# Kernel tuning notes

Measured on AMD Instinct MI355X. Metric: run time of the kernel, lower is better.

## Reference

```python
import jax, jax.numpy as jnp
import numpy as np

N_NODES = 10000
N_EDGES = 320000
D_FEAT = 128          # per-node feature dim -> in_dim = 2*D_FEAT = 256
OUT_DIM = 128
SCALES = 3


def setup_inputs() -> dict:
    key = jax.random.key(0)
    ks = jax.random.split(key, 7)
    node_features = jax.random.normal(ks[0], (N_NODES, D_FEAT), dtype=jnp.float32)
    temporal_info = jax.random.normal(ks[1], (N_NODES,), dtype=jnp.float32)
    in_dim_p1 = 2 * D_FEAT + 1  # 257: concat(src, dest) + temporal gap
    W1 = jax.random.normal(ks[2], (SCALES, in_dim_p1, OUT_DIM), dtype=jnp.float32) * 0.05
    b1 = jax.random.normal(ks[3], (SCALES, OUT_DIM), dtype=jnp.float32) * 0.05
    W2 = jax.random.normal(ks[4], (SCALES, OUT_DIM, OUT_DIM), dtype=jnp.float32) * 0.05
    b2 = jax.random.normal(ks[5], (SCALES, OUT_DIM), dtype=jnp.float32) * 0.05
    edge_index = jax.random.randint(ks[6], (2, N_EDGES), 0, N_NODES, dtype=jnp.int64)
    return {
        "node_features": node_features,
        "temporal_info": temporal_info,
        "W1": W1, "b1": b1, "W2": W2, "b2": b2,
        "edge_index": edge_index,
    }


def reference(node_features, temporal_info, W1, b1, W2, b2, edge_index):
    src, dest = edge_index[0], edge_index[1]
    # gather node pairs + temporal gap -> [E, 2*D+1]
    gap = (temporal_info[src] - temporal_info[dest])[:, None]
    edge_features = jnp.concatenate(
        [node_features[src], node_features[dest], gap], axis=-1)
    # all scales' 2-layer MLPs in one batched einsum; s = scale axis
    h = jax.nn.relu(jnp.einsum('ef,sfo->seo', edge_features, W1) + b1[:, None, :])
    tokens = jnp.einsum('seo,sop->sep', h, W2) + b2[:, None, :]  # [S, E, OUT]
    return tokens.mean(axis=0)  # mean over scales -> [E, OUT]
```

## Files before the change

### kernel.cpp

```cpp
#include <hip/hip_runtime.h>
#include <stdint.h>

#define NN 10000
#define NE 320000
#define DF 128
#define OD 128
#define NS 3

typedef __attribute__((ext_vector_type(8))) short bf16x8;
typedef __attribute__((ext_vector_type(16))) float f32x16;

static __device__ __forceinline__ uint32_t f2bf(float f) {
  uint32_t u = __float_as_uint(f);
  return (u + 0x7FFFu + ((u >> 16) & 1u)) >> 16;
}
static __device__ __forceinline__ float bflo(uint32_t u) { return __uint_as_float(u << 16); }
static __device__ __forceinline__ float bfhi(uint32_t u) { return __uint_as_float(u & 0xFFFF0000u); }

static __device__ __forceinline__ uint32_t relu2(uint32_t a, uint32_t d) {
  float f0 = fmaxf(bflo(a) + bflo(d), 0.0f);
  float f1 = fmaxf(bfhi(a) + bfhi(d), 0.0f);
  return f2bf(f0) | (f2bf(f1) << 16);
}

__global__ __launch_bounds__(256) void prep_w2(
    const float* __restrict__ W2, const float* __restrict__ b2,
    unsigned short* __restrict__ w2t, float* __restrict__ bmean)
{
  int tid = blockIdx.x * 256 + threadIdx.x;
  if (tid < NS * OD * OD) {
    int s = tid / (OD * OD);
    int r = tid % (OD * OD);
    int k = r / OD;
    int n = r % OD;
    w2t[(s * OD + n) * OD + k] = (unsigned short)f2bf(W2[tid]);
  }
  if (tid < OD) bmean[tid] = (b2[tid] + b2[OD + tid] + b2[2 * OD + tid]) * (1.0f / 3.0f);
}

__global__ __launch_bounds__(256) void node_proj(
    const float* __restrict__ nf, const float* __restrict__ temporal,
    const float* __restrict__ W1, const float* __restrict__ b1,
    unsigned short* __restrict__ Qsrc, unsigned short* __restrict__ Qdst)
{
  __shared__ unsigned short Asm[8 * 64 * 8];
  __shared__ unsigned short Bsm[4 * 8 * 64 * 8];
  __shared__ float tsh[32];

  const int t = threadIdx.x;
  const int c = blockIdx.y;
  const int s = c >> 1, proj = c & 1;

  {
    int o = t & 127, qh = t >> 7;
    const float* wbase = W1 + (size_t)(s * 257 + proj * 128) * OD + o;
    int nt = o >> 5, lnlo = o & 31;
    #pragma unroll
    for (int r = 0; r < 8; r++) {
      int kh = qh * 8 + r;
      float v[8];
      #pragma unroll
      for (int j = 0; j < 8; j++) v[j] = wbase[(size_t)(kh * 8 + j) * OD];
      uint32_t pk[4];
      #pragma unroll
      for (int i = 0; i < 4; i++) pk[i] = f2bf(v[2 * i]) | (f2bf(v[2 * i + 1]) << 16);
      int q = kh >> 1, half = kh & 1;
      uint32_t* d = (uint32_t*)(Bsm + ((nt * 8 + q) * 64 + half * 32 + lnlo) * 8);
      d[0] = pk[0]; d[1] = pk[1]; d[2] = pk[2]; d[3] = pk[3];
    }
  }

  const int lane = t & 63, w = t >> 6;
  const int o = w * 32 + (lane & 31);
  const float w1gv = W1[(size_t)(s * 257 + 256) * OD + o];
  const float b1v = b1[s * OD + o];
  unsigned short* Qt = (proj == 0) ? Qsrc : Qdst;
  const int m = t >> 3, j16 = t & 7;

  for (int it = 0; it < 8; it++) {
    const int m0 = (blockIdx.x * 8 + it) * 32;
    if (m0 >= NN) break;

    if (t < 32) tsh[t] = (m0 + t < NN) ? temporal[m0 + t] : 0.0f;

    {
      int node = m0 + m;
      float v[16];
      if (node < NN) {
        const float4* p = (const float4*)(nf + (size_t)node * DF + j16 * 16);
        #pragma unroll
        for (int i = 0; i < 4; i++) {
          float4 x = p[i];
          v[4 * i] = x.x; v[4 * i + 1] = x.y; v[4 * i + 2] = x.z; v[4 * i + 3] = x.w;
        }
      } else {
        #pragma unroll
        for (int i = 0; i < 16; i++) v[i] = 0.0f;
      }
      uint32_t pk[8];
      #pragma unroll
      for (int i = 0; i < 8; i++) pk[i] = f2bf(v[2 * i]) | (f2bf(v[2 * i + 1]) << 16);
      uint32_t* d0 = (uint32_t*)(Asm + (j16 * 64 + (m ^ j16)) * 8);
      uint32_t* d1 = (uint32_t*)(Asm + (j16 * 64 + ((32 + m) ^ j16)) * 8);
      d0[0] = pk[0]; d0[1] = pk[1]; d0[2] = pk[2]; d0[3] = pk[3];
      d1[0] = pk[4]; d1[1] = pk[5]; d1[2] = pk[6]; d1[3] = pk[7];
    }
    __syncthreads();

    f32x16 C;
    #pragma unroll
    for (int i = 0; i < 16; i++) C[i] = 0.0f;
    #pragma unroll
    for (int q = 0; q < 8; q++) {
      bf16x8 a = *(const bf16x8*)(Asm + (q * 64 + (lane ^ q)) * 8);
      bf16x8 b = *(const bf16x8*)(Bsm + ((w * 8 + q) * 64 + lane) * 8);
      C = __builtin_amdgcn_mfma_f32_32x32x16_bf16(a, b, C, 0, 0, 0);
    }

    #pragma unroll
    for (int r = 0; r < 16; r++) {
      int row = (r & 3) + 8 * (r >> 2) + 4 * (lane >> 5);
      int node = m0 + row;
      if (node < NN) {
        float val = C[r];
        if (proj == 0) val += b1v + tsh[row] * w1gv;
        else           val -= tsh[row] * w1gv;
        Qt[(size_t)node * (NS * OD) + s * OD + o] = (unsigned short)f2bf(val);
      }
    }
    __syncthreads();
  }
}

__global__ __launch_bounds__(256) void edge_mlp(
    const unsigned short* __restrict__ Qsrc, const unsigned short* __restrict__ Qdst,
    const unsigned short* __restrict__ W2T, const float* __restrict__ bmean,
    const int* __restrict__ ei, float* __restrict__ out)
{
  __shared__ unsigned short hsm[NS * 8 * 64 * 8];

  const int t = threadIdx.x;
  const int lane = t & 63, w = t >> 6;
  const int nlo = lane & 31, khi = lane >> 5;

  bf16x8 bfrag[NS][8];
  {
    int n = w * 32 + nlo;
    #pragma unroll
    for (int s = 0; s < NS; s++) {
      const unsigned short* base = W2T + ((s * OD + n) * OD + khi * 8);
      #pragma unroll
      for (int q = 0; q < 8; q++)
        bfrag[s][q] = *(const bf16x8*)(base + q * 16);
    }
  }
  const float bmv = bmean[w * 32 + nlo];

  const int m = t >> 3, j16 = t & 7;

  int sn[4], dn[4];
  #pragma unroll
  for (int tt = 0; tt < 4; tt++) {
    int e = blockIdx.x * 128 + tt * 32 + m;
    sn[tt] = ei[e];
    dn[tt] = ei[NE + e];
  }

  uint4 G[12], G2[12];
  {
    const unsigned short* ps = Qsrc + (size_t)sn[0] * (NS * OD) + j16 * 16;
    const unsigned short* pd = Qdst + (size_t)dn[0] * (NS * OD) + j16 * 16;
    #pragma unroll
    for (int s = 0; s < NS; s++) {
      G[4 * s + 0] = *(const uint4*)(ps + s * OD);
      G[4 * s + 1] = *(const uint4*)(ps + s * OD + 8);
      G[4 * s + 2] = *(const uint4*)(pd + s * OD);
      G[4 * s + 3] = *(const uint4*)(pd + s * OD + 8);
    }
  }

  #pragma unroll
  for (int tt = 0; tt < 4; tt++) {
    const int e0 = blockIdx.x * 128 + tt * 32;

    #pragma unroll
    for (int s = 0; s < NS; s++) {
      uint4 a0 = G[4 * s + 0], a1 = G[4 * s + 1];
      uint4 d0 = G[4 * s + 2], d1 = G[4 * s + 3];
      uint4 w0, w1;
      w0.x = relu2(a0.x, d0.x); w0.y = relu2(a0.y, d0.y);
      w0.z = relu2(a0.z, d0.z); w0.w = relu2(a0.w, d0.w);
      w1.x = relu2(a1.x, d1.x); w1.y = relu2(a1.y, d1.y);
      w1.z = relu2(a1.z, d1.z); w1.w = relu2(a1.w, d1.w);
      *(uint4*)(hsm + ((s * 8 + j16) * 64 + (m ^ j16)) * 8) = w0;
      *(uint4*)(hsm + ((s * 8 + j16) * 64 + ((32 + m) ^ j16)) * 8) = w1;
    }

    if (tt < 3) {
      const unsigned short* ps = Qsrc + (size_t)sn[tt + 1] * (NS * OD) + j16 * 16;
      const unsigned short* pd = Qdst + (size_t)dn[tt + 1] * (NS * OD) + j16 * 16;
      #pragma unroll
      for (int s = 0; s < NS; s++) {
        G2[4 * s + 0] = *(const uint4*)(ps + s * OD);
        G2[4 * s + 1] = *(const uint4*)(ps + s * OD + 8);
        G2[4 * s + 2] = *(const uint4*)(pd + s * OD);
        G2[4 * s + 3] = *(const uint4*)(pd + s * OD + 8);
      }
    }
    __syncthreads();

    f32x16 C;
    #pragma unroll
    for (int i = 0; i < 16; i++) C[i] = 0.0f;
    #pragma unroll
    for (int s = 0; s < NS; s++) {
      #pragma unroll
      for (int q = 0; q < 8; q++) {
        bf16x8 a = *(const bf16x8*)(hsm + ((s * 8 + q) * 64 + (lane ^ q)) * 8);
        C = __builtin_amdgcn_mfma_f32_32x32x16_bf16(a, bfrag[s][q], C, 0, 0, 0);
      }
    }

    #pragma unroll
    for (int r = 0; r < 16; r++) {
      int row = (r & 3) + 8 * (r >> 2) + 4 * khi;
      out[(size_t)(e0 + row) * OD + w * 32 + nlo] = C[r] * (1.0f / 3.0f) + bmv;
    }
    __syncthreads();

    #pragma unroll
    for (int i = 0; i < 12; i++) G[i] = G2[i];
  }
}

extern "C" void kernel_launch(void* const* d_in, const int* in_sizes, int n_in,
                              void* d_out, int out_size, void* d_ws, size_t ws_size,
                              hipStream_t stream) {
  const float* nf       = (const float*)d_in[0];
  const float* temporal = (const float*)d_in[1];
  const float* W1       = (const float*)d_in[2];
  const float* b1       = (const float*)d_in[3];
  const float* W2       = (const float*)d_in[4];
  const float* b2       = (const float*)d_in[5];
  const int*   ei       = (const int*)d_in[6];
  float* out = (float*)d_out;

  char* ws = (char*)d_ws;
  unsigned short* Qsrc = (unsigned short*)ws;
  unsigned short* Qdst = (unsigned short*)(ws + 7680000);
  unsigned short* W2T  = (unsigned short*)(ws + 15360000);
  float*          bmv  = (float*)(ws + 15360000 + 98304);

  prep_w2 <<<dim3(192),    dim3(256), 0, stream>>>(W2, b2, W2T, bmv);
  node_proj<<<dim3(40, 6), dim3(256), 0, stream>>>(nf, temporal, W1, b1, Qsrc, Qdst);
  edge_mlp <<<dim3(2500),  dim3(256), 0, stream>>>(Qsrc, Qdst, W2T, bmv, ei, out);
}
```

Measured before the change: 266.8 us.

## Bucket edges by source node range and schedule buckets per XCD for L2 locality

```diff
diff --git a/kernel.cpp b/kernel.cpp
--- a/kernel.cpp
+++ b/kernel.cpp
@@ -17,17 +17,21 @@
 static __device__ __forceinline__ float bflo(uint32_t u) { return __uint_as_float(u << 16); }
 static __device__ __forceinline__ float bfhi(uint32_t u) { return __uint_as_float(u & 0xFFFF0000u); }
 
-static __device__ __forceinline__ uint32_t relu2(uint32_t a, uint32_t d) {
+static __device__ __forceinline__ uint32_t relu2t(uint32_t a, uint32_t d) {
   float f0 = fmaxf(bflo(a) + bflo(d), 0.0f);
   float f1 = fmaxf(bfhi(a) + bfhi(d), 0.0f);
-  return f2bf(f0) | (f2bf(f1) << 16);
-}
+  return (__float_as_uint(f0) >> 16) | (__float_as_uint(f1) & 0xFFFF0000u);
+}
+
+static __device__ __forceinline__ int nbucket(int n) { return (n * 8) / NN; }
 
 __global__ __launch_bounds__(256) void prep_w2(
     const float* __restrict__ W2, const float* __restrict__ b2,
-    unsigned short* __restrict__ w2t, float* __restrict__ bmean)
+    unsigned short* __restrict__ w2t, float* __restrict__ bmean,
+    int* __restrict__ ctrl)
 {
   int tid = blockIdx.x * 256 + threadIdx.x;
+  if (blockIdx.x == 0) ctrl[threadIdx.x] = 0;
   if (tid < NS * OD * OD) {
     int s = tid / (OD * OD);
     int r = tid % (OD * OD);
@@ -36,6 +40,40 @@
     w2t[(s * OD + n) * OD + k] = (unsigned short)f2bf(W2[tid]);
   }
   if (tid < OD) bmean[tid] = (b2[tid] + b2[OD + tid] + b2[2 * OD + tid]) * (1.0f / 3.0f);
+}
+
+__global__ __launch_bounds__(256) void edge_hist(
+    const int* __restrict__ ei, int* __restrict__ ctrl)
+{
+  __shared__ int lh[64];
+  int t = threadIdx.x;
+  if (t < 64) lh[t] = 0;
+  __syncthreads();
+  int e = blockIdx.x * 256 + t;
+  int k = nbucket(ei[e]) * 8 + nbucket(ei[NE + e]);
+  atomicAdd(&lh[k], 1);
+  __syncthreads();
+  if (t < 64 && lh[t]) atomicAdd(&ctrl[t], lh[t]);
+}
+
+__global__ __launch_bounds__(64) void edge_scan(int* __restrict__ ctrl)
+{
+  if (threadIdx.x == 0) {
+    int acc = 0;
+    for (int i = 0; i < 64; i++) { ctrl[128 + i] = acc; acc += ctrl[i]; }
+    ctrl[128 + 64] = acc;
+    for (int x = 0; x < 8; x++) ctrl[200 + x] = ctrl[128 + 8 * x];
+    ctrl[208] = NE;
+  }
+}
+
+__global__ __launch_bounds__(256) void edge_scatter(
+    const int* __restrict__ ei, int* __restrict__ ctrl, int* __restrict__ perm)
+{
+  int e = blockIdx.x * 256 + threadIdx.x;
+  int k = nbucket(ei[e]) * 8 + nbucket(ei[NE + e]);
+  int pos = ctrl[128 + k] + atomicAdd(&ctrl[64 + k], 1);
+  perm[pos] = e;
 }
 
 __global__ __launch_bounds__(256) void node_proj(
@@ -135,9 +173,13 @@
 __global__ __launch_bounds__(256) void edge_mlp(
     const unsigned short* __restrict__ Qsrc, const unsigned short* __restrict__ Qdst,
     const unsigned short* __restrict__ W2T, const float* __restrict__ bmean,
-    const int* __restrict__ ei, float* __restrict__ out)
+    const int* __restrict__ ei, const int* __restrict__ perm,
+    const int* __restrict__ xcdStart, int* __restrict__ xcdCur,
+    float* __restrict__ out)
 {
   __shared__ unsigned short hsm[NS * 8 * 64 * 8];
+  __shared__ int psm[128];
+  __shared__ int chunkShared;
 
   const int t = threadIdx.x;
   const int lane = t & 63, w = t >> 6;
@@ -158,78 +200,102 @@
 
   const int m = t >> 3, j16 = t & 7;
 
-  int sn[4], dn[4];
-  #pragma unroll
-  for (int tt = 0; tt < 4; tt++) {
-    int e = blockIdx.x * 128 + tt * 32 + m;
-    sn[tt] = ei[e];
-    dn[tt] = ei[NE + e];
-  }
-
-  uint4 G[12], G2[12];
-  {
-    const unsigned short* ps = Qsrc + (size_t)sn[0] * (NS * OD) + j16 * 16;
-    const unsigned short* pd = Qdst + (size_t)dn[0] * (NS * OD) + j16 * 16;
-    #pragma unroll
-    for (int s = 0; s < NS; s++) {
-      G[4 * s + 0] = *(const uint4*)(ps + s * OD);
-      G[4 * s + 1] = *(const uint4*)(ps + s * OD + 8);
-      G[4 * s + 2] = *(const uint4*)(pd + s * OD);
-      G[4 * s + 3] = *(const uint4*)(pd + s * OD + 8);
-    }
-  }
-
-  #pragma unroll
-  for (int tt = 0; tt < 4; tt++) {
-    const int e0 = blockIdx.x * 128 + tt * 32;
-
-    #pragma unroll
-    for (int s = 0; s < NS; s++) {
-      uint4 a0 = G[4 * s + 0], a1 = G[4 * s + 1];
-      uint4 d0 = G[4 * s + 2], d1 = G[4 * s + 3];
-      uint4 w0, w1;
-      w0.x = relu2(a0.x, d0.x); w0.y = relu2(a0.y, d0.y);
-      w0.z = relu2(a0.z, d0.z); w0.w = relu2(a0.w, d0.w);
-      w1.x = relu2(a1.x, d1.x); w1.y = relu2(a1.y, d1.y);
-      w1.z = relu2(a1.z, d1.z); w1.w = relu2(a1.w, d1.w);
-      *(uint4*)(hsm + ((s * 8 + j16) * 64 + (m ^ j16)) * 8) = w0;
-      *(uint4*)(hsm + ((s * 8 + j16) * 64 + ((32 + m) ^ j16)) * 8) = w1;
-    }
-
-    if (tt < 3) {
-      const unsigned short* ps = Qsrc + (size_t)sn[tt + 1] * (NS * OD) + j16 * 16;
-      const unsigned short* pd = Qdst + (size_t)dn[tt + 1] * (NS * OD) + j16 * 16;
-      #pragma unroll
-      for (int s = 0; s < NS; s++) {
-        G2[4 * s + 0] = *(const uint4*)(ps + s * OD);
-        G2[4 * s + 1] = *(const uint4*)(ps + s * OD + 8);
-        G2[4 * s + 2] = *(const uint4*)(pd + s * OD);
-        G2[4 * s + 3] = *(const uint4*)(pd + s * OD + 8);
-      }
-    }
-    __syncthreads();
-
-    f32x16 C;
-    #pragma unroll
-    for (int i = 0; i < 16; i++) C[i] = 0.0f;
-    #pragma unroll
-    for (int s = 0; s < NS; s++) {
-      #pragma unroll
-      for (int q = 0; q < 8; q++) {
-        bf16x8 a = *(const bf16x8*)(hsm + ((s * 8 + q) * 64 + (lane ^ q)) * 8);
-        C = __builtin_amdgcn_mfma_f32_32x32x16_bf16(a, bfrag[s][q], C, 0, 0, 0);
-      }
-    }
-
-    #pragma unroll
-    for (int r = 0; r < 16; r++) {
-      int row = (r & 3) + 8 * (r >> 2) + 4 * khi;
-      out[(size_t)(e0 + row) * OD + w * 32 + nlo] = C[r] * (1.0f / 3.0f) + bmv;
-    }
-    __syncthreads();
-
-    #pragma unroll
-    for (int i = 0; i < 12; i++) G[i] = G2[i];
+  int myx;
+  asm volatile("s_getreg_b32 %0, hwreg(HW_REG_XCC_ID)" : "=s"(myx));
+  myx &= 7;
+
+  for (int qi = 0; qi < 8; qi++) {
+    const int q = (myx + qi) & 7;
+    const int S = xcdStart[q], E = xcdStart[q + 1];
+    const int tiles = (E - S + 127) >> 7;
+
+    while (true) {
+      if (t == 0) chunkShared = atomicAdd(&xcdCur[q], 1);
+      __syncthreads();
+      const int c128 = chunkShared;
+      __syncthreads();
+      if (c128 >= tiles) break;
+      const int base = S + (c128 << 7);
+
+      int sn[4], dn[4];
+      #pragma unroll
+      for (int tt = 0; tt < 4; tt++) {
+        int p = base + tt * 32 + m;
+        if (p >= E) p = E - 1;
+        int e = perm[p];
+        sn[tt] = ei[e];
+        dn[tt] = ei[NE + e];
+        if (j16 == 0) psm[tt * 32 + m] = e;
+      }
+
+      uint4 G[12], G2[12];
+      {
+        const unsigned short* ps = Qsrc + (size_t)sn[0] * (NS * OD) + j16 * 16;
+        const unsigned short* pd = Qdst + (size_t)dn[0] * (NS * OD) + j16 * 16;
+        #pragma unroll
+        for (int s = 0; s < NS; s++) {
+          G[4 * s + 0] = *(const uint4*)(ps + s * OD);
+          G[4 * s + 1] = *(const uint4*)(ps + s * OD + 8);
+          G[4 * s + 2] = *(const uint4*)(pd + s * OD);
+          G[4 * s + 3] = *(const uint4*)(pd + s * OD + 8);
+        }
+      }
+
+      #pragma unroll
+      for (int tt = 0; tt < 4; tt++) {
+        #pragma unroll
+        for (int s = 0; s < NS; s++) {
+          uint4 a0 = G[4 * s + 0], a1 = G[4 * s + 1];
+          uint4 d0 = G[4 * s + 2], d1 = G[4 * s + 3];
+          uint4 w0, w1;
+          w0.x = relu2t(a0.x, d0.x); w0.y = relu2t(a0.y, d0.y);
+          w0.z = relu2t(a0.z, d0.z); w0.w = relu2t(a0.w, d0.w);
+          w1.x = relu2t(a1.x, d1.x); w1.y = relu2t(a1.y, d1.y);
+          w1.z = relu2t(a1.z, d1.z); w1.w = relu2t(a1.w, d1.w);
+          *(uint4*)(hsm + ((s * 8 + j16) * 64 + (m ^ j16)) * 8) = w0;
+          *(uint4*)(hsm + ((s * 8 + j16) * 64 + ((32 + m) ^ j16)) * 8) = w1;
+        }
+
+        if (tt < 3) {
+          const unsigned short* ps = Qsrc + (size_t)sn[tt + 1] * (NS * OD) + j16 * 16;
+          const unsigned short* pd = Qdst + (size_t)dn[tt + 1] * (NS * OD) + j16 * 16;
+          #pragma unroll
+          for (int s = 0; s < NS; s++) {
+            G2[4 * s + 0] = *(const uint4*)(ps + s * OD);
+            G2[4 * s + 1] = *(const uint4*)(ps + s * OD + 8);
+            G2[4 * s + 2] = *(const uint4*)(pd + s * OD);
+            G2[4 * s + 3] = *(const uint4*)(pd + s * OD + 8);
+          }
+        }
+        __syncthreads();
+
+        f32x16 C;
+        #pragma unroll
+        for (int i = 0; i < 16; i++) C[i] = 0.0f;
+        #pragma unroll
+        for (int s = 0; s < NS; s++) {
+          #pragma unroll
+          for (int qq = 0; qq < 8; qq++) {
+            bf16x8 a = *(const bf16x8*)(hsm + ((s * 8 + qq) * 64 + (lane ^ qq)) * 8);
+            C = __builtin_amdgcn_mfma_f32_32x32x16_bf16(a, bfrag[s][qq], C, 0, 0, 0);
+          }
+        }
+
+        #pragma unroll
+        for (int r = 0; r < 16; r++) {
+          int row = (r & 3) + 8 * (r >> 2) + 4 * khi;
+          int pos = base + tt * 32 + row;
+          if (pos < E) {
+            int oe = psm[tt * 32 + row];
+            out[(size_t)oe * OD + w * 32 + nlo] = C[r] * (1.0f / 3.0f) + bmv;
+          }
+        }
+        __syncthreads();
+
+        #pragma unroll
+        for (int i = 0; i < 12; i++) G[i] = G2[i];
+      }
+    }
   }
 }
 
@@ -250,8 +316,14 @@
   unsigned short* Qdst = (unsigned short*)(ws + 7680000);
   unsigned short* W2T  = (unsigned short*)(ws + 15360000);
   float*          bmv  = (float*)(ws + 15360000 + 98304);
-
-  prep_w2 <<<dim3(192),    dim3(256), 0, stream>>>(W2, b2, W2T, bmv);
-  node_proj<<<dim3(40, 6), dim3(256), 0, stream>>>(nf, temporal, W1, b1, Qsrc, Qdst);
-  edge_mlp <<<dim3(2500),  dim3(256), 0, stream>>>(Qsrc, Qdst, W2T, bmv, ei, out);
-}
+  int*            ctrl = (int*)(ws + 15360000 + 98304 + 512);
+  int*            perm = (int*)(ws + 15360000 + 98304 + 512 + 1024);
+
+  prep_w2     <<<dim3(192),    dim3(256), 0, stream>>>(W2, b2, W2T, bmv, ctrl);
+  edge_hist   <<<dim3(1250),   dim3(256), 0, stream>>>(ei, ctrl);
+  edge_scan   <<<dim3(1),      dim3(64),  0, stream>>>(ctrl);
+  edge_scatter<<<dim3(1250),   dim3(256), 0, stream>>>(ei, ctrl, perm);
+  node_proj   <<<dim3(40, 6),  dim3(256), 0, stream>>>(nf, temporal, W1, b1, Qsrc, Qdst);
+  edge_mlp    <<<dim3(2500),   dim3(256), 0, stream>>>(Qsrc, Qdst, W2T, bmv, ei, perm,
+                                                       ctrl + 200, ctrl + 212, out);
+}
```

Measured after the change: 992.4 us. 272% more time.
